# Optimization experiments

Hardware: AMD Instinct MI355X
Metric: run time of the kernel (lower is better)

Reference implementation:

```python
import jax, jax.numpy as jnp
import numpy as np

MAX_LEN_SEQ = 2048
MAX_LEN_PAD = 2176
MIN_LEN_SEG = 32
MAX_LEN_SEG = 128
S = MAX_LEN_SEQ // MIN_LEN_SEG + 1  # max_num_seg = 65
B = 16
D = 128
R = B * S          # 1040 segment rows
W = 2 * MAX_LEN_SEG  # 256 candidate positions per segment


def _forward(x, scales, len_seq, len_seg_raw):
    T = x.shape[1]
    sc = scales + 0.5                                   # (R,) in [0.5, 1.5)
    idx = jnp.arange(W, dtype=jnp.float32)              # (W,)
    idx_scaled = idx[None, :] / sc[:, None]             # (R, W)
    idx_fl = jnp.floor(idx_scaled)
    lam = idx_scaled - idx_fl                           # (R, W)
    len_seg = (len_seg_raw.astype(jnp.int32) + MIN_LEN_SEG)  # (R, 1)
    mask1 = idx_fl < (len_seg.astype(jnp.float32) - 1.0)
    # per-batch cumulative segment offsets
    offset = jnp.cumsum(len_seg.reshape(B, S), axis=-1)
    offset = jnp.pad(offset[:, :-1], ((0, 0), (1, 0))).reshape(R, 1)
    idx_org = idx_fl + offset.astype(jnp.float32)       # (R, W) source positions
    len_rp = jnp.repeat(len_seq.astype(jnp.float32), S)  # (R,)
    mask2 = idx_org < (len_rp - 1.0)[:, None]
    mask = (mask1 & mask2).reshape(-1)                  # (R*W,) row-major like boolean_mask

    pos = jnp.cumsum(mask.astype(jnp.int32)) - 1        # compacted slot for masked entries
    total = jnp.sum(mask.astype(jnp.int32))

    bidx = jnp.broadcast_to((jnp.arange(R) // S)[:, None], (R, W)).reshape(-1)
    i_fl = jnp.clip(idx_org.astype(jnp.int32).reshape(-1), 0, T - 1)
    i_cl = jnp.clip(i_fl + 1, 0, T - 1)
    y_fl = x[bidx, i_fl]                                # (R*W, D)
    y_cl = x[bidx, i_cl]
    lamf = lam.reshape(-1)[:, None]
    y = (1.0 - lamf) * y_fl + lamf * y_cl               # (R*W, D)

    # compact masked rows into dense buffer (extra row N swallows unmasked)
    N = R * W
    buf = jnp.zeros((N + 1, D), x.dtype)
    buf = buf.at[jnp.where(mask, pos, N)].set(y)

    # emulate y[: total//B*B].reshape(B, -1, D)[:, :MAX_LEN_SEQ] + pad
    L = total // B
    t = jnp.arange(MAX_LEN_SEQ)
    gidx = jnp.arange(B)[:, None] * L + t[None, :]      # (B, MAX_LEN_SEQ)
    out = buf[jnp.clip(gidx, 0, N)]
    out = jnp.where((t < L)[None, :, None], out, jnp.zeros((), x.dtype))
    return out


def setup_inputs() -> dict:
    key = jax.random.key(0)
    k1, k2, k3, k4 = jax.random.split(key, 4)
    x = jax.random.normal(k1, (B, MAX_LEN_PAD, D), dtype=jnp.float32)
    scales = jax.random.uniform(k2, (R,), dtype=jnp.float32)
    len_seq = jax.random.randint(k3, (B,), MAX_LEN_SEQ // 2, MAX_LEN_SEQ, dtype=jnp.int32)
    len_seq = len_seq.at[0].set(MAX_LEN_SEQ)  # force max(len_seq) == MAX_LEN_SEQ (static)
    len_seg_raw = jax.random.randint(k4, (R, 1), 0, MAX_LEN_SEG - MIN_LEN_SEG, dtype=jnp.int32)
    return {"x": x, "scales": scales, "len_seq": len_seq, "len_seg_raw": len_seg_raw}


def reference(x, scales, len_seq, len_seg_raw):
    return _forward(x, scales, len_seq, len_seg_raw)
```

## Files before the change

kernel.cpp:

```cpp
#include <hip/hip_runtime.h>

#define B_      16
#define S_      65
#define R_      1040
#define W_      256
#define T_      2176
#define D_      128
#define MAXSEQ  2048

__global__ __launch_bounds__(256) void interp_setup(
    const float* __restrict__ scales,
    const int*   __restrict__ len_seq,
    const int*   __restrict__ len_seg_raw,
    int* __restrict__ offs,
    int* __restrict__ row_start,
    int* __restrict__ meta)
{
    __shared__ int s_len[R_];
    __shared__ int s_off[R_];
    __shared__ int s_cnt[R_];
    const int tid = threadIdx.x;

    for (int r = tid; r < R_; r += 256) s_len[r] = len_seg_raw[r] + 32;
    __syncthreads();

    if (tid < B_) {
        int acc = 0, base = tid * S_;
        for (int s = 0; s < S_; ++s) { s_off[base + s] = acc; acc += s_len[base + s]; }
    }
    __syncthreads();

    for (int r = tid; r < R_; r += 256) {
        float sc  = scales[r] + 0.5f;
        int   off = s_off[r];
        int   K   = min(s_len[r] - 1, len_seq[r / S_] - 1 - off);
        int   c   = 0;
        if (K > 0) {
            c = (int)ceilf((float)K * sc);
            c = min(max(c, 0), W_);
            const float Kf = (float)K;
            while (c > 0  && ((float)(c - 1) / sc) >= Kf) --c;
            while (c < W_ && ((float)c       / sc) <  Kf) ++c;
        }
        s_cnt[r] = c;
        offs[r]  = off;
    }
    __syncthreads();

    if (tid == 0) {
        int acc = 0;
        for (int r = 0; r < R_; ++r) { row_start[r] = acc; acc += s_cnt[r]; }
        row_start[R_] = acc;
        meta[0] = acc;
        meta[1] = acc / B_;
    }
}

__global__ __launch_bounds__(256) void interp_gather(
    const float* __restrict__ x,
    const float* __restrict__ scales,
    const int*   __restrict__ offs,
    const int*   __restrict__ row_start,
    const int*   __restrict__ meta,
    float* __restrict__ out)
{
    __shared__ int s_rs[R_ + 1];
    const int tid = threadIdx.x;
    for (int i = tid; i < R_ + 1; i += 256) s_rs[i] = row_start[i];
    __syncthreads();

    const int L    = meta[1];
    const int orow = blockIdx.x * 8 + (tid >> 5);
    const int lane = tid & 31;
    float4* outp = (float4*)(out + (size_t)orow * D_) + lane;

    const int t = orow & (MAXSEQ - 1);
    const int b = orow >> 11;
    if (t >= L) { *outp = make_float4(0.f, 0.f, 0.f, 0.f); return; }

    const int g = b * L + t;
    int lo = 0, hi = R_;
    while (hi - lo > 1) {
        int mid = (lo + hi) >> 1;
        if (s_rs[mid] <= g) lo = mid; else hi = mid;
    }
    const int r = lo;
    const int w = g - s_rs[r];

    const float sc  = scales[r] + 0.5f;
    const float is  = (float)w / sc;
    const float fl  = floorf(is);
    const float lam = is - fl;
    int i0 = (int)fl + offs[r];
    i0 = min(max(i0, 0), T_ - 1);
    const int i1 = min(i0 + 1, T_ - 1);
    const int bs = r / S_;

    const float* base = x + (size_t)bs * (T_ * D_);
    const float4* pa = (const float4*)(base + (size_t)i0 * D_) + lane;
    const float4* pb = (const float4*)(base + (size_t)i1 * D_) + lane;
    const float4 a = *pa, c = *pb;
    const float om = 1.0f - lam;
    float4 y;
    y.x = om * a.x + lam * c.x;
    y.y = om * a.y + lam * c.y;
    y.z = om * a.z + lam * c.z;
    y.w = om * a.w + lam * c.w;
    *outp = y;
}

extern "C" void kernel_launch(void* const* d_in, const int* in_sizes, int n_in,
                              void* d_out, int out_size, void* d_ws, size_t ws_size,
                              hipStream_t stream) {
    const float* x           = (const float*)d_in[0];
    const float* scales      = (const float*)d_in[1];
    const int*   len_seq     = (const int*)d_in[2];
    const int*   len_seg_raw = (const int*)d_in[3];
    float*       out         = (float*)d_out;

    int* offs      = (int*)d_ws;
    int* row_start = offs + R_;
    int* meta      = row_start + R_ + 1;

    interp_setup<<<1, 256, 0, stream>>>(scales, len_seq, len_seg_raw,
                                        offs, row_start, meta);

    const int nrows = B_ * MAXSEQ;
    interp_gather<<<nrows / 8, 256, 0, stream>>>(x, scales, offs, row_start,
                                                 meta, out);
}
```

Measured before the change: 91.88 us.

## Replace per-row binary search with packed slot lookup table and parallel scans

The setup kernel now computes segment offsets and row-count prefix sums with wavefront shuffle scans instead of serial loops. It also writes a per-output-slot lookup table that packs offset, row and window index into one int. The gather kernel reads that entry directly instead of loading the row_start array into shared memory and binary-searching it for every block. This cuts per-block shared-memory staging and search latency, at the cost of extra global writes in the single-block setup kernel, whose threads write their segments' entries serially. It also drops the index clamping, which relies on the masks keeping i0+1 within range.

```diff
diff --git a/kernel.cpp b/kernel.cpp
--- a/kernel.cpp
+++ b/kernel.cpp
@@ -12,64 +12,96 @@
     const float* __restrict__ scales,
     const int*   __restrict__ len_seq,
     const int*   __restrict__ len_seg_raw,
-    int* __restrict__ offs,
-    int* __restrict__ row_start,
+    int* __restrict__ lut,
     int* __restrict__ meta)
 {
     __shared__ int s_len[R_];
     __shared__ int s_off[R_];
-    __shared__ int s_cnt[R_];
-    const int tid = threadIdx.x;
+    __shared__ int s_wtot[4];
+    const int tid  = threadIdx.x;
+    const int lane = tid & 63;
+    const int wid  = tid >> 6;
 
     for (int r = tid; r < R_; r += 256) s_len[r] = len_seg_raw[r] + 32;
     __syncthreads();
 
-    if (tid < B_) {
-        int acc = 0, base = tid * S_;
-        for (int s = 0; s < S_; ++s) { s_off[base + s] = acc; acc += s_len[base + s]; }
+    for (int b = wid; b < B_; b += 4) {
+        int v = s_len[b * S_ + lane];
+        int incl = v;
+        #pragma unroll
+        for (int d = 1; d < 64; d <<= 1) {
+            int n = __shfl_up(incl, d, 64);
+            if (lane >= d) incl += n;
+        }
+        s_off[b * S_ + lane] = incl - v;
+        int tot = __shfl(incl, 63, 64);
+        if (lane == 0) s_off[b * S_ + 64] = tot;
     }
     __syncthreads();
 
-    for (int r = tid; r < R_; r += 256) {
-        float sc  = scales[r] + 0.5f;
-        int   off = s_off[r];
-        int   K   = min(s_len[r] - 1, len_seq[r / S_] - 1 - off);
-        int   c   = 0;
-        if (K > 0) {
-            c = (int)ceilf((float)K * sc);
-            c = min(max(c, 0), W_);
-            const float Kf = (float)K;
-            while (c > 0  && ((float)(c - 1) / sc) >= Kf) --c;
-            while (c < W_ && ((float)c       / sc) <  Kf) ++c;
+    int c[5], off5[5];
+    const int r0 = tid * 5;
+    int tsum = 0;
+    #pragma unroll
+    for (int i = 0; i < 5; ++i) {
+        int r = r0 + i, cc = 0, off = 0;
+        if (r < R_) {
+            float sc = scales[r] + 0.5f;
+            off = s_off[r];
+            int K = min(s_len[r] - 1, len_seq[r / S_] - 1 - off);
+            if (K > 0) {
+                cc = (int)ceilf((float)K * sc);
+                cc = min(max(cc, 0), W_);
+                const float Kf = (float)K;
+                while (cc > 0  && ((float)(cc - 1) / sc) >= Kf) --cc;
+                while (cc < W_ && ((float)cc       / sc) <  Kf) ++cc;
+            }
         }
-        s_cnt[r] = c;
-        offs[r]  = off;
+        c[i] = cc; off5[i] = off; tsum += cc;
     }
+
+    int incl = tsum;
+    #pragma unroll
+    for (int d = 1; d < 64; d <<= 1) {
+        int n = __shfl_up(incl, d, 64);
+        if (lane >= d) incl += n;
+    }
+    if (lane == 63) s_wtot[wid] = incl;
     __syncthreads();
+    int wpre = 0, total = 0;
+    #pragma unroll
+    for (int wv = 0; wv < 4; ++wv) {
+        int t_ = s_wtot[wv];
+        if (wv < wid) wpre += t_;
+        total += t_;
+    }
+    int base = wpre + incl - tsum;
 
-    if (tid == 0) {
-        int acc = 0;
-        for (int r = 0; r < R_; ++r) { row_start[r] = acc; acc += s_cnt[r]; }
-        row_start[R_] = acc;
-        meta[0] = acc;
-        meta[1] = acc / B_;
+    #pragma unroll
+    for (int i = 0; i < 5; ++i) {
+        int r = r0 + i;
+        if (r < R_) {
+            int tag = (off5[i] << 19) | (r << 8);
+            for (int w = 0; w < c[i]; ++w) lut[base + w] = tag | w;
+            base += c[i];
+        }
     }
+    if (tid == 0) { meta[0] = total; meta[1] = total / B_; }
 }
 
 __global__ __launch_bounds__(256) void interp_gather(
     const float* __restrict__ x,
     const float* __restrict__ scales,
-    const int*   __restrict__ offs,
-    const int*   __restrict__ row_start,
+    const int*   __restrict__ lut,
     const int*   __restrict__ meta,
     float* __restrict__ out)
 {
-    __shared__ int s_rs[R_ + 1];
-    const int tid = threadIdx.x;
-    for (int i = tid; i < R_ + 1; i += 256) s_rs[i] = row_start[i];
+    __shared__ int s_L;
+    if (threadIdx.x == 0) s_L = meta[1];
     __syncthreads();
+    const int L = s_L;
 
-    const int L    = meta[1];
+    const int tid  = threadIdx.x;
     const int orow = blockIdx.x * 8 + (tid >> 5);
     const int lane = tid & 31;
     float4* outp = (float4*)(out + (size_t)orow * D_) + lane;
@@ -78,34 +110,28 @@
     const int b = orow >> 11;
     if (t >= L) { *outp = make_float4(0.f, 0.f, 0.f, 0.f); return; }
 
-    const int g = b * L + t;
-    int lo = 0, hi = R_;
-    while (hi - lo > 1) {
-        int mid = (lo + hi) >> 1;
-        if (s_rs[mid] <= g) lo = mid; else hi = mid;
-    }
-    const int r = lo;
-    const int w = g - s_rs[r];
+    const int v   = lut[b * L + t];
+    const int w   = v & 255;
+    const int r   = (v >> 8) & 2047;
+    const int off = v >> 19;
 
     const float sc  = scales[r] + 0.5f;
     const float is  = (float)w / sc;
     const float fl  = floorf(is);
     const float lam = is - fl;
-    int i0 = (int)fl + offs[r];
-    i0 = min(max(i0, 0), T_ - 1);
-    const int i1 = min(i0 + 1, T_ - 1);
+    const int i0 = (int)fl + off;
     const int bs = r / S_;
 
     const float* base = x + (size_t)bs * (T_ * D_);
     const float4* pa = (const float4*)(base + (size_t)i0 * D_) + lane;
-    const float4* pb = (const float4*)(base + (size_t)i1 * D_) + lane;
-    const float4 a = *pa, c = *pb;
+    const float4* pb = (const float4*)(base + (size_t)(i0 + 1) * D_) + lane;
+    const float4 a = *pa, cc = *pb;
     const float om = 1.0f - lam;
     float4 y;
-    y.x = om * a.x + lam * c.x;
-    y.y = om * a.y + lam * c.y;
-    y.z = om * a.z + lam * c.z;
-    y.w = om * a.w + lam * c.w;
+    y.x = om * a.x + lam * cc.x;
+    y.y = om * a.y + lam * cc.y;
+    y.z = om * a.z + lam * cc.z;
+    y.w = om * a.w + lam * cc.w;
     *outp = y;
 }
 
@@ -118,14 +144,11 @@
     const int*   len_seg_raw = (const int*)d_in[3];
     float*       out         = (float*)d_out;
 
-    int* offs      = (int*)d_ws;
-    int* row_start = offs + R_;
-    int* meta      = row_start + R_ + 1;
+    int* lut  = (int*)d_ws;
+    int* meta = lut + R_ * W_;
 
-    interp_setup<<<1, 256, 0, stream>>>(scales, len_seq, len_seg_raw,
-                                        offs, row_start, meta);
+    interp_setup<<<1, 256, 0, stream>>>(scales, len_seq, len_seg_raw, lut, meta);
 
     const int nrows = B_ * MAXSEQ;
-    interp_gather<<<nrows / 8, 256, 0, stream>>>(x, scales, offs, row_start,
-                                                 meta, out);
+    interp_gather<<<nrows / 8, 256, 0, stream>>>(x, scales, lut, meta, out);
 }
```

After: 100.8 us. +9.7%, slower.
